# Optimization experiments

Measured on AMD Instinct MI355X. Metric: run time of the kernel, lower is better.

## Reference

```python
import jax, jax.numpy as jnp
import numpy as np

N_NODES = 50000
N_EDGES = 800000
D = 128
H = 8
HD = D // H
N_NTYPES = 3
N_ETYPES = 5
LN_EPS = 1e-5


def setup_inputs() -> dict:
    key = jax.random.key(0)
    ks = jax.random.split(key, 16)
    inp = {
        "x": jax.random.normal(ks[0], (N_NODES, D), dtype=jnp.float32),
        "edge_index": jax.random.randint(ks[1], (2, N_EDGES), 0, N_NODES),
        "edge_type": jax.random.randint(ks[2], (N_EDGES,), 0, N_ETYPES),
        "node_type": jax.random.randint(ks[3], (N_NODES,), 0, N_NTYPES),
        # per-(node_type, head) QKV projections, per-(edge_type, head) K transform
        "W_Q": jax.random.normal(ks[4], (N_NTYPES, H, HD, HD), dtype=jnp.float32) * 0.02,
        "W_K": jax.random.normal(ks[5], (N_NTYPES, H, HD, HD), dtype=jnp.float32) * 0.02,
        "W_V": jax.random.normal(ks[6], (N_NTYPES, H, HD, HD), dtype=jnp.float32) * 0.02,
        "W_edge": jax.random.normal(ks[7], (N_ETYPES, H, HD, HD), dtype=jnp.float32) * 0.02,
        "mu": jnp.ones((H, N_ETYPES), dtype=jnp.float32),
        "W_out": jax.random.normal(ks[8], (D, D), dtype=jnp.float32) * 0.02,
        "b_out": jnp.zeros((D,), dtype=jnp.float32),
        "ln1_g": jnp.ones((D,), dtype=jnp.float32),
        "ln1_b": jnp.zeros((D,), dtype=jnp.float32),
        "W1": jax.random.normal(ks[9], (D, 4 * D), dtype=jnp.float32) * 0.02,
        "b1": jnp.zeros((4 * D,), dtype=jnp.float32),
        "W2": jax.random.normal(ks[10], (4 * D, D), dtype=jnp.float32) * 0.02,
        "b2": jnp.zeros((D,), dtype=jnp.float32),
        "ln2_g": jnp.ones((D,), dtype=jnp.float32),
        "ln2_b": jnp.zeros((D,), dtype=jnp.float32),
    }
    return inp


def _layer_norm(y, g, b):
    m = y.mean(-1, keepdims=True)
    v = ((y - m) ** 2).mean(-1, keepdims=True)
    return (y - m) * jax.lax.rsqrt(v + LN_EPS) * g + b


def reference(x, edge_index, edge_type, node_type,
              W_Q, W_K, W_V, W_edge, mu,
              W_out, b_out, ln1_g, ln1_b, W1, b1, W2, b2, ln2_g, ln2_b):
    N = x.shape[0]
    xh = x.reshape(N, H, HD)  # heads vectorized (concat of per-head slices)

    # type-specific QKV: small fixed loop over node types, masked select
    Q = jnp.zeros_like(xh)
    K = jnp.zeros_like(xh)
    V = jnp.zeros_like(xh)
    for t in range(N_NTYPES):
        m = (node_type == t)[:, None, None]
        Q = jnp.where(m, jnp.einsum('nhd,hdf->nhf', xh, W_Q[t]), Q)
        K = jnp.where(m, jnp.einsum('nhd,hdf->nhf', xh, W_K[t]), K)
        V = jnp.where(m, jnp.einsum('nhd,hdf->nhf', xh, W_V[t]), V)

    src, dst = edge_index[0], edge_index[1]
    q_dst = Q[dst]   # [E,H,HD]
    k_src = K[src]   # [E,H,HD]

    # edge-type-specific K transform
    kt = jnp.zeros_like(k_src)
    for et in range(N_ETYPES):
        m = (edge_type == et)[:, None, None]
        kt = jnp.where(m, jnp.einsum('ehd,hdf->ehf', k_src, W_edge[et]), kt)

    scores = (q_dst * kt).sum(-1) / jnp.sqrt(jnp.float32(HD))  # [E,H]
    scores = scores * mu[:, edge_type].T                       # mu per edge type, per head

    # sparse softmax over incoming edges of each dst node, per head
    smax = jax.ops.segment_max(scores, dst, num_segments=N)
    ex = jnp.exp(scores - smax[dst])
    den = jax.ops.segment_sum(ex, dst, num_segments=N)
    w = ex / (den[dst] + 1e-10)                                 # [E,H]

    agg = jax.ops.segment_sum(V[src] * w[..., None], dst, num_segments=N)  # [N,H,HD]
    mh = agg.reshape(N, D) @ W_out + b_out  # dropout is identity in eval

    h = _layer_norm(x + mh, ln1_g, ln1_b)
    ffn = jax.nn.gelu(h @ W1 + b1, approximate=False) @ W2 + b2
    return _layer_norm(h + ffn, ln2_g, ln2_b)
```

## Files before the change

### kernel.cpp

```cpp
#include <hip/hip_runtime.h>
#include <hip/hip_bf16.h>

#define N_NODESC 50000
#define N_EDGESC 800000
#define DD 128
#define HH 8
#define HDIM 16
#define N_NT 3
#define N_ET 5
#define NPB 196
#define NEB 400
#define NFB 512

#define KV8_OFF    ((size_t)0)
#define QT8_OFF    ((size_t)12800000)
#define XP_OFF     ((size_t)44800000)
#define AGG_OFF    ((size_t)57600000)
#define WOUTT_OFF  ((size_t)83200000)
#define W1T_OFF    ((size_t)83232768)
#define W2T_OFF    ((size_t)83363840)
#define WALL_OFF   ((size_t)83494912)
#define EDATA_OFF  ((size_t)84183040)
#define ROWS_OFF   ((size_t)87383040)
#define ORIG_OFF   ((size_t)87583104)
#define DEG_OFF    ((size_t)87783104)
#define TOFS_OFF   ((size_t)87983104)
#define BH_OFF     ((size_t)87983168)
#define BB_OFF     ((size_t)87985536)
#define TMP_OFF    ((size_t)87988928)
#define RLOC_OFF   ((size_t)91188928)
#define CSUM_OFF   ((size_t)91389056)

using short8 = __attribute__((ext_vector_type(8))) short;
using f32x4  = __attribute__((ext_vector_type(4))) float;
using f32x2  = __attribute__((ext_vector_type(2))) float;

__device__ __forceinline__ ushort f2b(float f) {
    __hip_bfloat16 h = __float2bfloat16(f);
    return *(ushort*)&h;
}
__device__ __forceinline__ float b2f(ushort u) {
    __hip_bfloat16 h = *(__hip_bfloat16*)&u;
    return __bfloat162float(h);
}
__device__ __forceinline__ f32x2 pk0(unsigned int w) {
    return __builtin_amdgcn_cvt_pk_f32_fp8((int)w, false);
}
__device__ __forceinline__ f32x2 pk1(unsigned int w) {
    return __builtin_amdgcn_cvt_pk_f32_fp8((int)w, true);
}
__device__ __forceinline__ float gelu_f(float v) {
    return 0.5f * v * (1.f + erff(v * 0.70710678118654752f));
}
__device__ __forceinline__ void ebar() {
    __builtin_amdgcn_sched_barrier(0);
    asm volatile("s_waitcnt lgkmcnt(0)" ::: "memory");
    __builtin_amdgcn_sched_barrier(0);
    __builtin_amdgcn_s_barrier();
    __builtin_amdgcn_sched_barrier(0);
}

__global__ __launch_bounds__(256) void prep_a(
    const float* __restrict__ Wout, const float* __restrict__ W1, const float* __restrict__ W2,
    const float* __restrict__ WQ, const float* __restrict__ Wk, const float* __restrict__ Wv,
    const float* __restrict__ We, const float* __restrict__ mu,
    ushort* __restrict__ Woutt, ushort* __restrict__ W1t, ushort* __restrict__ W2t,
    ushort* __restrict__ Wall,
    const int* __restrict__ ntype, int* __restrict__ bh,
    const int* __restrict__ dst, int* __restrict__ deg, unsigned int* __restrict__ tmp)
{
    const int b = blockIdx.x, tid = threadIdx.x;
    if (b < 1920) {
        const int gid = b * 256 + tid;
        if (gid < 16384) {
            const int nn = gid >> 7, k = gid & 127;
            Woutt[gid] = f2b(Wout[k * 128 + nn]);
        } else if (gid < 81920) {
            const int i = gid - 16384;
            const int nn = i >> 7, k = i & 127;
            W1t[i] = f2b(W1[k * 512 + nn]);
        } else if (gid < 147456) {
            const int i = gid - 81920;
            const int nn = i >> 9, k = i & 511;
            W2t[i] = f2b(W2[k * 128 + nn]);
        } else {
            const int idx = gid - 147456;
            const int t = idx / (896 * 128);
            const int rem = idx % (896 * 128);
            const int c = rem / 128, k = rem % 128;
            const int hk = k >> 4, ck = k & 15;
            float v = 0.f;
            if (c < 128) {
                const int hc = c >> 4, j = c & 15;
                if (hk == hc) v = 4.f * Wk[((t * HH + hc) * HDIM + ck) * HDIM + j];
            } else if (c < 256) {
                const int c2 = c - 128, hc = c2 >> 4, j = c2 & 15;
                if (hk == hc) v = 4.f * Wv[((t * HH + hc) * HDIM + ck) * HDIM + j];
            } else {
                const int cq = c - 256, et = cq >> 7, dd = cq & 127;
                const int hq = dd >> 4, j = dd & 15;
                if (hk == hq) {
                    const float* wq = WQ + ((t * HH + hq) * HDIM + ck) * HDIM;
                    const float* we = We + ((et * HH + hq) * HDIM + j) * HDIM;
                    float s = 0.f;
#pragma unroll
                    for (int f = 0; f < 16; f++) s = fmaf(wq[f], we[f], s);
                    v = 64.f * mu[hq * N_ET + et] * s;
                }
            }
            Wall[idx] = f2b(v);
        }
    } else if (b < 1920 + NPB) {
        const int bc = b - 1920;
        const int wave = tid >> 6, lane = tid & 63;
        const int n = bc * 256 + tid;
        const int t = (n < N_NODESC) ? ntype[n] : -1;
        const unsigned long long m0 = __ballot(t == 0);
        const unsigned long long m1 = __ballot(t == 1);
        const unsigned long long m2 = __ballot(t == 2);
        __shared__ int wcnt[4][3];
        if (lane == 0) {
            wcnt[wave][0] = (int)__popcll(m0);
            wcnt[wave][1] = (int)__popcll(m1);
            wcnt[wave][2] = (int)__popcll(m2);
        }
        __syncthreads();
        if (tid < 3)
            bh[tid * NPB + bc] = wcnt[0][tid] + wcnt[1][tid] + wcnt[2][tid] + wcnt[3][tid];
    } else {
        for (int e = (b - 1920 - NPB) * 256 + tid; e < N_EDGESC; e += NEB * 256) {
            const int nd = dst[e];
            const unsigned int p = (unsigned int)atomicAdd(&deg[nd], 1);
            tmp[e] = (p << 16) | (unsigned int)nd;
        }
    }
}

__global__ __launch_bounds__(256) void prep_b(
    const int* __restrict__ bh, const int* __restrict__ deg,
    int* __restrict__ bb, int* __restrict__ tofs,
    int* __restrict__ rloc, int* __restrict__ csum)
{
    __shared__ int part[256];
    const int tid = threadIdx.x;
    if (blockIdx.x == 0) {
        const int base3 = tid * 3;
        int e0 = (base3 + 0 < 588) ? bh[base3 + 0] : 0;
        int e1 = (base3 + 1 < 588) ? bh[base3 + 1] : 0;
        int e2 = (base3 + 2 < 588) ? bh[base3 + 2] : 0;
        const int l0 = e0, l1 = e0 + e1, l2 = l1 + e2;
        part[tid] = l2;
        __syncthreads();
        for (int off = 1; off < 256; off <<= 1) {
            const int u = (tid >= off) ? part[tid - off] : 0;
            __syncthreads();
            part[tid] += u;
            __syncthreads();
        }
        const int tb = part[tid] - l2;
        if (base3 + 0 < 588) bb[base3 + 0] = tb;
        if (base3 + 1 < 588) bb[base3 + 1] = tb + l0;
        if (base3 + 2 < 588) bb[base3 + 2] = tb + l1;
        __syncthreads();
        if (tid == 0) {
            tofs[0] = 0;
            tofs[1] = bb[NPB];
            tofs[2] = bb[2 * NPB];
            tofs[3] = N_NODESC;
        }
    } else {
        const int c = blockIdx.x - 1;
        const int n = c * 256 + tid;
        const int vdeg = (n < N_NODESC) ? deg[n] : 0;
        part[tid] = vdeg;
        __syncthreads();
        for (int off = 1; off < 256; off <<= 1) {
            const int u = (tid >= off) ? part[tid - off] : 0;
            __syncthreads();
            part[tid] += u;
            __syncthreads();
        }
        if (n <= N_NODESC) rloc[n] = part[tid] - vdeg;
        if (tid == 255) csum[c] = part[255];
    }
}

__global__ __launch_bounds__(256) void prep_c(
    const int* __restrict__ ntype, const float* __restrict__ x,
    const int* __restrict__ src, const int* __restrict__ etype,
    const int* __restrict__ bb, const int* __restrict__ rloc, const int* __restrict__ csum,
    const unsigned int* __restrict__ tmp,
    int* __restrict__ origof, ushort* __restrict__ Xp, int* __restrict__ rows,
    int* __restrict__ edata)
{
    const int b = blockIdx.x, tid = threadIdx.x;
    __shared__ int cb[256];
    {
        const int v = (tid < NPB) ? csum[tid] : 0;
        cb[tid] = v;
        __syncthreads();
        for (int off = 1; off < 256; off <<= 1) {
            const int u = (tid >= off) ? cb[tid - off] : 0;
            __syncthreads();
            cb[tid] += u;
            __syncthreads();
        }
        const int incl = cb[tid];
        __syncthreads();
        cb[tid] = incl - v;
        __syncthreads();
    }

    if (b < NPB) {
        const int wave = tid >> 6, lane = tid & 63;
        const int n = b * 256 + tid;
        const int t = (n < N_NODESC) ? ntype[n] : -1;
        const unsigned long long m0 = __ballot(t == 0);
        const unsigned long long m1 = __ballot(t == 1);
        const unsigned long long m2 = __ballot(t == 2);
        __shared__ int wcnt[4][3];
        __shared__ int sp[256];
        if (lane == 0) {
            wcnt[wave][0] = (int)__popcll(m0);
            wcnt[wave][1] = (int)__popcll(m1);
            wcnt[wave][2] = (int)__popcll(m2);
        }
        __syncthreads();
        int p = -1;
        if (n < N_NODESC) {
            int basew = 0;
#pragma unroll
            for (int w = 0; w < 4; w++) if (w < wave) basew += wcnt[w][t];
            const unsigned long long mt = (t == 0) ? m0 : (t == 1) ? m1 : m2;
            const unsigned long long mlt = ((unsigned long long)1 << lane) - 1;
            p = bb[t * NPB + b] + basew + (int)__popcll(mt & mlt);
            origof[p] = n;
        }
        if (n <= N_NODESC) rows[n] = cb[b] + rloc[n];
        sp[tid] = p;
        __syncthreads();
        for (int i = tid; i < 256 * 16; i += 256) {
            const int nn = i >> 4, c = (i & 15) << 3;
            const int pp = sp[nn];
            if (pp < 0) continue;
            const int n2 = b * 256 + nn;
            const float4 v0 = *(const float4*)(x + (size_t)n2 * DD + c);
            const float4 v1 = *(const float4*)(x + (size_t)n2 * DD + c + 4);
            ushort o[8] = {f2b(v0.x), f2b(v0.y), f2b(v0.z), f2b(v0.w),
                           f2b(v1.x), f2b(v1.y), f2b(v1.z), f2b(v1.w)};
            *(uint4*)(Xp + (size_t)pp * DD + c) = *(uint4*)o;
        }
    } else {
        for (int e = (b - NPB) * 256 + tid; e < N_EDGESC; e += NFB * 256) {
            const unsigned int v = tmp[e];
            const int nd = (int)(v & 0xffffu);
            const int p = (int)(v >> 16);
            edata[cb[nd >> 8] + rloc[nd] + p] = src[e] | (etype[e] << 16);
        }
    }
}

#define LDP 36

__global__ __launch_bounds__(256) void proj_gemm(
    const ushort* __restrict__ Xp, const ushort* __restrict__ Wall,
    const int* __restrict__ tofs, const int* __restrict__ origof,
    ushort* __restrict__ KV8, unsigned char* __restrict__ Qt8)
{
    const int t = blockIdx.z;
    const int rs = tofs[t], re = tofs[t + 1];
    const int mBase = rs + blockIdx.x * 128;
    if (mBase >= re) return;
    const int nBase = blockIdx.y * 128;
    const ushort* Bt = Wall + (size_t)t * 896 * 128;

    __shared__ ushort As[128 * LDP];
    __shared__ ushort Bs[128 * LDP];
    const int tid = threadIdx.x;
    const int lane = tid & 63, wave = tid >> 6;
    const int mw = (wave >> 1) * 64, nw = (wave & 1) * 64;
    const int l15 = lane & 15, q8 = (lane >> 4) * 8;

    f32x4 acc[4][4];
#pragma unroll
    for (int i = 0; i < 4; i++)
#pragma unroll
        for (int j = 0; j < 4; j++) acc[i][j] = (f32x4){0.f, 0.f, 0.f, 0.f};

    const int r0 = tid >> 2, c0 = (tid & 3) * 8;
    int rA0 = mBase + r0;      if (rA0 >= N_NODESC) rA0 = N_NODESC - 1;
    int rA1 = mBase + r0 + 64; if (rA1 >= N_NODESC) rA1 = N_NODESC - 1;

    for (int kk = 0; kk < 128; kk += 32) {
        short8 a0 = *(const short8*)(Xp + (size_t)rA0 * DD + kk + c0);
        short8 a1 = *(const short8*)(Xp + (size_t)rA1 * DD + kk + c0);
        short8 b0 = *(const short8*)(Bt + (size_t)(nBase + r0) * 128 + kk + c0);
        short8 b1 = *(const short8*)(Bt + (size_t)(nBase + r0 + 64) * 128 + kk + c0);
        *(short8*)&As[r0 * LDP + c0] = a0;
        *(short8*)&As[(r0 + 64) * LDP + c0] = a1;
        *(short8*)&Bs[r0 * LDP + c0] = b0;
        *(short8*)&Bs[(r0 + 64) * LDP + c0] = b1;
        __syncthreads();
        short8 af[4], bf[4];
#pragma unroll
        for (int i = 0; i < 4; i++)
            af[i] = *(const short8*)&As[(mw + i * 16 + l15) * LDP + q8];
#pragma unroll
        for (int j = 0; j < 4; j++)
            bf[j] = *(const short8*)&Bs[(nw + j * 16 + l15) * LDP + q8];
#pragma unroll
        for (int i = 0; i < 4; i++)
#pragma unroll
            for (int j = 0; j < 4; j++)
                acc[i][j] = __builtin_amdgcn_mfma_f32_16x16x32_bf16(af[i], bf[j], acc[i][j], 0, 0, 0);
        __syncthreads();
    }

    unsigned char* kvb = (unsigned char*)KV8;
    const int rq = (lane >> 4) * 4;
#pragma unroll
    for (int i = 0; i < 4; i++) {
#pragma unroll
        for (int r = 0; r < 4; r++) {
            const int gm = mBase + mw + i * 16 + rq + r;
            if (gm >= re) continue;
            const int og = origof[gm];
#pragma unroll
            for (int j = 0; j < 4; j++) {
                const int gn = nBase + nw + j * 16 + l15;
                const float v = acc[i][j][r];
                const unsigned char b8 =
                    (unsigned char)(__builtin_amdgcn_cvt_pk_fp8_f32(v, v, 0, false) & 0xff);
                if (gn < 256) kvb[(size_t)og * 256 + gn] = b8;
                else          Qt8[(size_t)og * 640 + (gn - 256)] = b8;
            }
        }
    }
}

__global__ __launch_bounds__(128) void edgeagg_kernel(
    const int* __restrict__ rowstart, const int* __restrict__ edata,
    const unsigned char* __restrict__ Qt8, const unsigned char* __restrict__ KV8,
    ushort* __restrict__ agg)
{
    const int w = threadIdx.x >> 6;
    const int lane = threadIdx.x & 63;
    const int n = blockIdx.x * 2 + w;
    const int slot = lane >> 3;
    const int h = lane & 7;

    __shared__ uint4 qs8s[2][40];
    if (lane < 40)
        qs8s[w][lane] = ((const uint4*)(Qt8 + (size_t)n * 640))[lane];
    __syncthreads();
    const uint* qbase = (const uint*)&qs8s[w][0];

    const int s0 = rowstart[n], s1 = rowstart[n + 1];
    const float qsc = 1.44269504f / 1024.f;

    float acc[16];
#pragma unroll
    for (int j = 0; j < 16; j++) acc[j] = 0.f;
    float den = 0.f;

    for (int i = s0 + slot; i < s1; i += 8) {
        const int ed = edata[i];
        const int sn = ed & 0xffff;
        const int et = ed >> 16;
        const unsigned char* kvp = KV8 + ((size_t)sn << 8);
        const uint4 kw = *(const uint4*)(kvp + (h << 4));
        const uint4 vw = *(const uint4*)(kvp + 128 + (h << 4));
        const uint4 qw = *(const uint4*)(qbase + (et << 5) + (h << 2));

        const f32x2 q0 = pk0(qw.x), q1 = pk1(qw.x), q2 = pk0(qw.y), q3 = pk1(qw.y);
        const f32x2 q4 = pk0(qw.z), q5 = pk1(qw.z), q6 = pk0(qw.w), q7 = pk1(qw.w);
        const f32x2 k0 = pk0(kw.x), k1 = pk1(kw.x), k2 = pk0(kw.y), k3 = pk1(kw.y);
        const f32x2 k4 = pk0(kw.z), k5 = pk1(kw.z), k6 = pk0(kw.w), k7 = pk1(kw.w);

        float pa = q0.x * k0.x;
        float pb = q0.y * k0.y;
        float pc = q1.x * k1.x;
        float pd = q1.y * k1.y;
        pa = fmaf(q2.x, k2.x, pa); pb = fmaf(q2.y, k2.y, pb);
        pc = fmaf(q3.x, k3.x, pc); pd = fmaf(q3.y, k3.y, pd);
        pa = fmaf(q4.x, k4.x, pa); pb = fmaf(q4.y, k4.y, pb);
        pc = fmaf(q5.x, k5.x, pc); pd = fmaf(q5.y, k5.y, pd);
        pa = fmaf(q6.x, k6.x, pa); pb = fmaf(q6.y, k6.y, pb);
        pc = fmaf(q7.x, k7.x, pc); pd = fmaf(q7.y, k7.y, pd);

        const float ex = exp2f(((pa + pb) + (pc + pd)) * qsc);
        den += ex;

        const f32x2 v0 = pk0(vw.x), v1 = pk1(vw.x), v2 = pk0(vw.y), v3 = pk1(vw.y);
        const f32x2 v4 = pk0(vw.z), v5 = pk1(vw.z), v6 = pk0(vw.w), v7 = pk1(vw.w);
        acc[0]  = fmaf(ex, v0.x, acc[0]);  acc[1]  = fmaf(ex, v0.y, acc[1]);
        acc[2]  = fmaf(ex, v1.x, acc[2]);  acc[3]  = fmaf(ex, v1.y, acc[3]);
        acc[4]  = fmaf(ex, v2.x, acc[4]);  acc[5]  = fmaf(ex, v2.y, acc[5]);
        acc[6]  = fmaf(ex, v3.x, acc[6]);  acc[7]  = fmaf(ex, v3.y, acc[7]);
        acc[8]  = fmaf(ex, v4.x, acc[8]);  acc[9]  = fmaf(ex, v4.y, acc[9]);
        acc[10] = fmaf(ex, v5.x, acc[10]); acc[11] = fmaf(ex, v5.y, acc[11]);
        acc[12] = fmaf(ex, v6.x, acc[12]); acc[13] = fmaf(ex, v6.y, acc[13]);
        acc[14] = fmaf(ex, v7.x, acc[14]); acc[15] = fmaf(ex, v7.y, acc[15]);
    }

    {
        const int b0 = slot & 1, b1 = slot & 2, b2 = slot & 4;
#pragma unroll
        for (int j = 0; j < 8; j++) {
            const float v = b0 ? acc[j] : acc[j + 8];
            const float r = __shfl_xor(v, 8);
            acc[j] = (b0 ? acc[j + 8] : acc[j]) + r;
        }
#pragma unroll
        for (int j = 0; j < 4; j++) {
            const float v = b1 ? acc[j] : acc[j + 4];
            const float r = __shfl_xor(v, 16);
            acc[j] = (b1 ? acc[j + 4] : acc[j]) + r;
        }
#pragma unroll
        for (int j = 0; j < 2; j++) {
            const float v = b2 ? acc[j] : acc[j + 2];
            const float r = __shfl_xor(v, 32);
            acc[j] = (b2 ? acc[j + 2] : acc[j]) + r;
        }
        den += __shfl_xor(den, 8);
        den += __shfl_xor(den, 16);
        den += __shfl_xor(den, 32);
    }
    const float rr = 0.25f / (den + 1e-10f);
    const int fb = (h << 4) + ((slot & 1) << 3) + ((slot & 2) << 1) + ((slot & 4) >> 1);
    ushort o2[2] = { f2b(acc[0] * rr), f2b(acc[1] * rr) };
    *(uint*)&agg[((size_t)n << 7) + fb] = *(uint*)o2;
}

#define LDH 132
#define LDB 132

__global__ __launch_bounds__(256) void fused_tail(
    const ushort* __restrict__ agg, const ushort* __restrict__ Woutt,
    const ushort* __restrict__ W1t, const ushort* __restrict__ W2t,
    const float* __restrict__ x,
    const float* __restrict__ bout, const float* __restrict__ g1, const float* __restrict__ b1ln,
    const float* __restrict__ b1, const float* __restrict__ b2,
    const float* __restrict__ g2, const float* __restrict__ b2ln,
    float* __restrict__ out)
{
    __shared__ ushort Bs[128 * LDB];
    __shared__ ushort Hs[64 * LDH];
    __shared__ ushort Ts[64 * LDH];
    __shared__ float red[2][2][64];

    const int tid = threadIdx.x;
    const int lane = tid & 63, wave = tid >> 6;
    const int wm = wave >> 1, wn = wave & 1;
    const int l15 = lane & 15, q8 = (lane >> 4) * 8, rq = (lane >> 4) * 4;
    const int mBase = blockIdx.x * 64;

    const int r0 = tid >> 2, c0 = (tid & 3) * 8;
    int rowA = mBase + r0; if (rowA >= N_NODESC) rowA = N_NODESC - 1;

    short8 pA[4], pB0[4], pB1[4];
#pragma unroll
    for (int kk = 0; kk < 4; kk++) {
        pA[kk]  = *(const short8*)(agg + (size_t)rowA * DD + kk * 32 + c0);
        pB0[kk] = *(const short8*)(Woutt + (size_t)r0 * 128 + kk * 32 + c0);
        pB1[kk] = *(const short8*)(Woutt + (size_t)(r0 + 64) * 128 + kk * 32 + c0);
    }
    float xv[2][4][4];
#pragma unroll
    for (int i = 0; i < 2; i++)
#pragma unroll
        for (int r = 0; r < 4; r++) {
            const int gm = mBase + wm * 32 + i * 16 + rq + r;
            const int gr = (gm < N_NODESC) ? gm : N_NODESC - 1;
#pragma unroll
            for (int j = 0; j < 4; j++)
                xv[i][r][j] = x[(size_t)gr * DD + wn * 64 + j * 16 + l15];
        }

    f32x4 acc1[2][4], acc2[2][4];
#pragma unroll
    for (int i = 0; i < 2; i++)
#pragma unroll
        for (int j = 0; j < 4; j++) {
            acc1[i][j] = (f32x4){0.f, 0.f, 0.f, 0.f};
            acc2[i][j] = (f32x4){0.f, 0.f, 0.f, 0.f};
        }

#pragma unroll
    for (int kk = 0; kk < 4; kk++) {
        *(short8*)&Ts[r0 * LDH + kk * 32 + c0] = pA[kk];
        *(short8*)&Bs[r0 * LDB + kk * 32 + c0] = pB0[kk];
        *(short8*)&Bs[(r0 + 64) * LDB + kk * 32 + c0] = pB1[kk];
    }
#pragma unroll
    for (int kk = 0; kk < 4; kk++) {
        pB0[kk] = *(const short8*)(W1t + (size_t)r0 * 128 + kk * 32 + c0);
        pB1[kk] = *(const short8*)(W1t + (size_t)(r0 + 64) * 128 + kk * 32 + c0);
    }
    ebar();
#pragma unroll
    for (int kk = 0; kk < 4; kk++) {
        short8 af[2], bf[4];
#pragma unroll
        for (int i = 0; i < 2; i++)
            af[i] = *(const short8*)&Ts[(wm * 32 + i * 16 + l15) * LDH + kk * 32 + q8];
#pragma unroll
        for (int j = 0; j < 4; j++)
            bf[j] = *(const short8*)&Bs[(wn * 64 + j * 16 + l15) * LDB + kk * 32 + q8];
#pragma unroll
        for (int i = 0; i < 2; i++)
#pragma unroll
            for (int j = 0; j < 4; j++)
                acc1[i][j] = __builtin_amdgcn_mfma_f32_16x16x32_bf16(af[i], bf[j], acc1[i][j], 0, 0, 0);
    }

    {
        float boutv[4], gv[4], bv[4];
#pragma unroll
        for (int j = 0; j < 4; j++) {
            const int gn = wn * 64 + j * 16 + l15;
            boutv[j] = bout[gn]; gv[j] = g1[gn]; bv[j] = b1ln[gn];
        }
#pragma unroll
        for (int i = 0; i < 2; i++) {
#pragma unroll
            for (int r = 0; r < 4; r++) {
                const int row = wm * 32 + i * 16 + rq + r;
                float s = 0.f, ss = 0.f;
#pragma unroll
                for (int j = 0; j < 4; j++) {
                    float v = acc1[i][j][r] + boutv[j] + xv[i][r][j];
                    acc1[i][j][r] = v;
                    s += v; ss += v * v;
                }
                s  += __shfl_xor(s, 1);  s  += __shfl_xor(s, 2);  s  += __shfl_xor(s, 4);  s  += __shfl_xor(s, 8);
                ss += __shfl_xor(ss, 1); ss += __shfl_xor(ss, 2); ss += __shfl_xor(ss, 4); ss += __shfl_xor(ss, 8);
                if (l15 == 0) { red[0][wn][row] = s; red[1][wn][row] = ss; }
            }
        }
        ebar();
#pragma unroll
        for (int i = 0; i < 2; i++) {
#pragma unroll
            for (int r = 0; r < 4; r++) {
                const int row = wm * 32 + i * 16 + rq + r;
                const float s  = red[0][0][row] + red[0][1][row];
                const float ss = red[1][0][row] + red[1][1][row];
                const float mean = s * (1.f / 128.f);
                const float var  = ss * (1.f / 128.f) - mean * mean;
                const float rstd = rsqrtf(var + 1e-5f);
#pragma unroll
                for (int j = 0; j < 4; j++) {
                    const int gn = wn * 64 + j * 16 + l15;
                    Hs[row * LDH + gn] = f2b((acc1[i][j][r] - mean) * rstd * gv[j] + bv[j]);
                }
            }
        }
    }

    for (int nb = 0; nb < 4; nb++) {
        ebar();
#pragma unroll
        for (int kk = 0; kk < 4; kk++) {
            *(short8*)&Bs[r0 * LDB + kk * 32 + c0] = pB0[kk];
            *(short8*)&Bs[(r0 + 64) * LDB + kk * 32 + c0] = pB1[kk];
        }
#pragma unroll
        for (int kk = 0; kk < 4; kk++) {
            pB0[kk] = *(const short8*)(W2t + (size_t)r0 * 512 + nb * 128 + kk * 32 + c0);
            pB1[kk] = *(const short8*)(W2t + (size_t)(r0 + 64) * 512 + nb * 128 + kk * 32 + c0);
        }
        ebar();
        f32x4 a1[2][4];
#pragma unroll
        for (int i = 0; i < 2; i++)
#pragma unroll
            for (int j = 0; j < 4; j++) a1[i][j] = (f32x4){0.f, 0.f, 0.f, 0.f};
#pragma unroll
        for (int kk = 0; kk < 4; kk++) {
            short8 af[2], bf[4];
#pragma unroll
            for (int i = 0; i < 2; i++)
                af[i] = *(const short8*)&Hs[(wm * 32 + i * 16 + l15) * LDH + kk * 32 + q8];
#pragma unroll
            for (int j = 0; j < 4; j++)
                bf[j] = *(const short8*)&Bs[(wn * 64 + j * 16 + l15) * LDB + kk * 32 + q8];
#pragma unroll
            for (int i = 0; i < 2; i++)
#pragma unroll
                for (int j = 0; j < 4; j++)
                    a1[i][j] = __builtin_amdgcn_mfma_f32_16x16x32_bf16(af[i], bf[j], a1[i][j], 0, 0, 0);
        }

        ebar();
        {
            float b1v[4];
#pragma unroll
            for (int j = 0; j < 4; j++)
                b1v[j] = b1[nb * 128 + wn * 64 + j * 16 + l15];
#pragma unroll
            for (int i = 0; i < 2; i++)
#pragma unroll
                for (int j = 0; j < 4; j++)
#pragma unroll
                    for (int r = 0; r < 4; r++) {
                        const int row = wm * 32 + i * 16 + rq + r;
                        const int col = wn * 64 + j * 16 + l15;
                        Ts[row * LDH + col] = f2b(gelu_f(a1[i][j][r] + b1v[j]));
                    }
        }
#pragma unroll
        for (int kk = 0; kk < 4; kk++) {
            *(short8*)&Bs[r0 * LDB + kk * 32 + c0] = pB0[kk];
            *(short8*)&Bs[(r0 + 64) * LDB + kk * 32 + c0] = pB1[kk];
        }
        if (nb < 3) {
#pragma unroll
            for (int kk = 0; kk < 4; kk++) {
                pB0[kk] = *(const short8*)(W1t + (size_t)((nb + 1) * 128 + r0) * 128 + kk * 32 + c0);
                pB1[kk] = *(const short8*)(W1t + (size_t)((nb + 1) * 128 + r0 + 64) * 128 + kk * 32 + c0);
            }
        }
        ebar();
#pragma unroll
        for (int kk = 0; kk < 4; kk++) {
            short8 af[2], bf[4];
#pragma unroll
            for (int i = 0; i < 2; i++)
                af[i] = *(const short8*)&Ts[(wm * 32 + i * 16 + l15) * LDH + kk * 32 + q8];
#pragma unroll
            for (int j = 0; j < 4; j++)
                bf[j] = *(const short8*)&Bs[(wn * 64 + j * 16 + l15) * LDB + kk * 32 + q8];
#pragma unroll
            for (int i = 0; i < 2; i++)
#pragma unroll
                for (int j = 0; j < 4; j++)
                    acc2[i][j] = __builtin_amdgcn_mfma_f32_16x16x32_bf16(af[i], bf[j], acc2[i][j], 0, 0, 0);
        }
    }

    {
        float b2v[4], gv[4], bv[4];
#pragma unroll
        for (int j = 0; j < 4; j++) {
            const int gn = wn * 64 + j * 16 + l15;
            b2v[j] = b2[gn]; gv[j] = g2[gn]; bv[j] = b2ln[gn];
        }
#pragma unroll
        for (int i = 0; i < 2; i++) {
#pragma unroll
            for (int r = 0; r < 4; r++) {
                const int row = wm * 32 + i * 16 + rq + r;
                float s = 0.f, ss = 0.f;
#pragma unroll
                for (int j = 0; j < 4; j++) {
                    const int gn = wn * 64 + j * 16 + l15;
                    float v = acc2[i][j][r] + b2v[j] + b2f(Hs[row * LDH + gn]);
                    acc2[i][j][r] = v;
                    s += v; ss += v * v;
                }
                s  += __shfl_xor(s, 1);  s  += __shfl_xor(s, 2);  s  += __shfl_xor(s, 4);  s  += __shfl_xor(s, 8);
                ss += __shfl_xor(ss, 1); ss += __shfl_xor(ss, 2); ss += __shfl_xor(ss, 4); ss += __shfl_xor(ss, 8);
                if (l15 == 0) { red[0][wn][row] = s; red[1][wn][row] = ss; }
            }
        }
        ebar();
#pragma unroll
        for (int i = 0; i < 2; i++) {
#pragma unroll
            for (int r = 0; r < 4; r++) {
                const int row = wm * 32 + i * 16 + rq + r;
                const int gm = mBase + row;
                if (gm >= N_NODESC) continue;
                const float s  = red[0][0][row] + red[0][1][row];
                const float ss = red[1][0][row] + red[1][1][row];
                const float mean = s * (1.f / 128.f);
                const float var  = ss * (1.f / 128.f) - mean * mean;
                const float rstd = rsqrtf(var + 1e-5f);
#pragma unroll
                for (int j = 0; j < 4; j++) {
                    const int gn = wn * 64 + j * 16 + l15;
                    out[(size_t)gm * DD + gn] = (acc2[i][j][r] - mean) * rstd * gv[j] + bv[j];
                }
            }
        }
    }
}

extern "C" void kernel_launch(void* const* d_in, const int* in_sizes, int n_in,
                              void* d_out, int out_size, void* d_ws, size_t ws_size,
                              hipStream_t stream)
{
    const float* x     = (const float*)d_in[0];
    const int*   ei    = (const int*)d_in[1];
    const int*   etyp  = (const int*)d_in[2];
    const int*   ntype = (const int*)d_in[3];
    const float* Wq    = (const float*)d_in[4];
    const float* Wk    = (const float*)d_in[5];
    const float* Wv    = (const float*)d_in[6];
    const float* We    = (const float*)d_in[7];
    const float* mu    = (const float*)d_in[8];
    const float* Wout  = (const float*)d_in[9];
    const float* bout  = (const float*)d_in[10];
    const float* g1    = (const float*)d_in[11];
    const float* b1ln  = (const float*)d_in[12];
    const float* W1    = (const float*)d_in[13];
    const float* b1    = (const float*)d_in[14];
    const float* W2    = (const float*)d_in[15];
    const float* b2    = (const float*)d_in[16];
    const float* g2    = (const float*)d_in[17];
    const float* b2ln  = (const float*)d_in[18];
    float* out = (float*)d_out;

    char* ws = (char*)d_ws;
    ushort*        KV8   = (ushort*)(ws + KV8_OFF);
    unsigned char* Qt8   = (unsigned char*)(ws + QT8_OFF);
    ushort*        Xp    = (ushort*)(ws + XP_OFF);
    ushort*        agg   = (ushort*)(ws + AGG_OFF);
    ushort*        Woutt = (ushort*)(ws + WOUTT_OFF);
    ushort*        W1t   = (ushort*)(ws + W1T_OFF);
    ushort*        W2t   = (ushort*)(ws + W2T_OFF);
    ushort*        Wall  = (ushort*)(ws + WALL_OFF);
    int*           edata = (int*)(ws + EDATA_OFF);
    int*           rows  = (int*)(ws + ROWS_OFF);
    int*           origof= (int*)(ws + ORIG_OFF);
    int*           deg   = (int*)(ws + DEG_OFF);
    int*           tofs  = (int*)(ws + TOFS_OFF);
    int*           bh    = (int*)(ws + BH_OFF);
    int*           bb    = (int*)(ws + BB_OFF);
    unsigned int*  tmp   = (unsigned int*)(ws + TMP_OFF);
    int*           rloc  = (int*)(ws + RLOC_OFF);
    int*           csum  = (int*)(ws + CSUM_OFF);

    const int* srcA = ei;
    const int* dstA = ei + N_EDGESC;

    (void)hipMemsetAsync(ws + DEG_OFF, 0, 200000, stream);

    prep_a<<<1920 + NPB + NEB, 256, 0, stream>>>(
        Wout, W1, W2, Wq, Wk, Wv, We, mu, Woutt, W1t, W2t, Wall,
        ntype, bh, dstA, deg, tmp);
    prep_b<<<1 + NPB, 256, 0, stream>>>(bh, deg, bb, tofs, rloc, csum);
    prep_c<<<NPB + NFB, 256, 0, stream>>>(ntype, x, srcA, etyp, bb, rloc, csum, tmp,
                                          origof, Xp, rows, edata);

    proj_gemm<<<dim3(394, 7, 3), 256, 0, stream>>>(Xp, Wall, tofs, origof, KV8, Qt8);
    edgeagg_kernel<<<N_NODESC / 2, 128, 0, stream>>>(rows, edata, Qt8,
                                                     (const unsigned char*)KV8, agg);

    fused_tail<<<782, 256, 0, stream>>>(agg, Woutt, W1t, W2t, x,
                                        bout, g1, b1ln, b1, b2, g2, b2ln, out);
}
```

Baseline: 317.7 us.

## Restructure fused tail to 512 threads with K-split double-buffered weights and fast GELU

The fused tail kernel moves from 4 to 8 waves per block, each wave handling a 32x32 output tile. The weight tiles are split into two 64-wide K halves held in a double-buffered LDS array, so global loads of the next half can overlap the MFMA work on the current one. The exact erff in GELU is replaced by an Abramowitz-Stegun polynomial using a hardware reciprocal and a fast exp. This trades extra barriers and an approximation error of about 1e-7 in erf for better latency hiding and occupancy.

```diff
diff --git a/kernel.cpp b/kernel.cpp
--- a/kernel.cpp
+++ b/kernel.cpp
@@ -50,7 +50,20 @@
     return __builtin_amdgcn_cvt_pk_f32_fp8((int)w, true);
 }
 __device__ __forceinline__ float gelu_f(float v) {
-    return 0.5f * v * (1.f + erff(v * 0.70710678118654752f));
+    const float x = v * 0.70710678118654752f;
+    const float ax = fabsf(x);
+    const float d = fmaf(0.3275911f, ax, 1.0f);
+    float t;
+    asm("v_rcp_f32 %0, %1" : "=v"(t) : "v"(d));
+    float p = fmaf(1.061405429f, t, -1.453152027f);
+    p = fmaf(p, t, 1.421413741f);
+    p = fmaf(p, t, -0.284496736f);
+    p = fmaf(p, t, 0.254829592f);
+    p = p * t;
+    const float e = __expf(-ax * ax);
+    const float er = 1.0f - p * e;
+    const float erfx = (x < 0.f) ? -er : er;
+    return 0.5f * v * (1.0f + erfx);
 }
 __device__ __forceinline__ void ebar() {
     __builtin_amdgcn_sched_barrier(0);
@@ -434,9 +447,13 @@
 }
 
 #define LDH 132
-#define LDB 132
-
-__global__ __launch_bounds__(256) void fused_tail(
+#define LDB2 68
+
+#define LOADB(P0, P1, PTR) { P0 = *(const short8*)(PTR); P1 = *(const short8*)((PTR) + 8); }
+#define STAGEB(BUF, P0, P1) { *(short8*)&Bs[BUF][br * LDB2 + bc] = P0; \
+                              *(short8*)&Bs[BUF][br * LDB2 + bc + 8] = P1; }
+
+__global__ __launch_bounds__(512, 4) void fused_tail(
     const ushort* __restrict__ agg, const ushort* __restrict__ Woutt,
     const ushort* __restrict__ W1t, const ushort* __restrict__ W2t,
     const float* __restrict__ x,
@@ -445,28 +462,36 @@
     const float* __restrict__ g2, const float* __restrict__ b2ln,
     float* __restrict__ out)
 {
-    __shared__ ushort Bs[128 * LDB];
+    __shared__ ushort Bs[2][128 * LDB2];
     __shared__ ushort Hs[64 * LDH];
     __shared__ ushort Ts[64 * LDH];
-    __shared__ float red[2][2][64];
+    __shared__ float red[2][4][64];
 
     const int tid = threadIdx.x;
     const int lane = tid & 63, wave = tid >> 6;
-    const int wm = wave >> 1, wn = wave & 1;
+    const int wm = wave >> 2, wn = wave & 3;
     const int l15 = lane & 15, q8 = (lane >> 4) * 8, rq = (lane >> 4) * 4;
     const int mBase = blockIdx.x * 64;
 
-    const int r0 = tid >> 2, c0 = (tid & 3) * 8;
-    int rowA = mBase + r0; if (rowA >= N_NODESC) rowA = N_NODESC - 1;
-
-    short8 pA[4], pB0[4], pB1[4];
-#pragma unroll
-    for (int kk = 0; kk < 4; kk++) {
-        pA[kk]  = *(const short8*)(agg + (size_t)rowA * DD + kk * 32 + c0);
-        pB0[kk] = *(const short8*)(Woutt + (size_t)r0 * 128 + kk * 32 + c0);
-        pB1[kk] = *(const short8*)(Woutt + (size_t)(r0 + 64) * 128 + kk * 32 + c0);
-    }
-    float xv[2][4][4];
+    const int br = tid >> 2, bc = (tid & 3) * 16;
+    const int ar = tid >> 3, ac = (tid & 7) * 16;
+    int rowA = mBase + ar; if (rowA >= N_NODESC) rowA = N_NODESC - 1;
+
+    f32x4 acc1[2][2], acc2[2][2];
+#pragma unroll
+    for (int i = 0; i < 2; i++)
+#pragma unroll
+        for (int j = 0; j < 2; j++) {
+            acc1[i][j] = (f32x4){0.f, 0.f, 0.f, 0.f};
+            acc2[i][j] = (f32x4){0.f, 0.f, 0.f, 0.f};
+        }
+
+    short8 pX0, pX1, pY0, pY1, aT0, aT1;
+    LOADB(pX0, pX1, Woutt + (size_t)br * 128 + bc);
+    LOADB(pY0, pY1, Woutt + (size_t)br * 128 + 64 + bc);
+    aT0 = *(const short8*)(agg + (size_t)rowA * DD + ac);
+    aT1 = *(const short8*)(agg + (size_t)rowA * DD + ac + 8);
+    float xv[2][4][2];
 #pragma unroll
     for (int i = 0; i < 2; i++)
 #pragma unroll
@@ -474,53 +499,59 @@
             const int gm = mBase + wm * 32 + i * 16 + rq + r;
             const int gr = (gm < N_NODESC) ? gm : N_NODESC - 1;
 #pragma unroll
-            for (int j = 0; j < 4; j++)
-                xv[i][r][j] = x[(size_t)gr * DD + wn * 64 + j * 16 + l15];
-        }
-
-    f32x4 acc1[2][4], acc2[2][4];
-#pragma unroll
-    for (int i = 0; i < 2; i++)
-#pragma unroll
-        for (int j = 0; j < 4; j++) {
-            acc1[i][j] = (f32x4){0.f, 0.f, 0.f, 0.f};
-            acc2[i][j] = (f32x4){0.f, 0.f, 0.f, 0.f};
-        }
-
-#pragma unroll
-    for (int kk = 0; kk < 4; kk++) {
-        *(short8*)&Ts[r0 * LDH + kk * 32 + c0] = pA[kk];
-        *(short8*)&Bs[r0 * LDB + kk * 32 + c0] = pB0[kk];
-        *(short8*)&Bs[(r0 + 64) * LDB + kk * 32 + c0] = pB1[kk];
-    }
-#pragma unroll
-    for (int kk = 0; kk < 4; kk++) {
-        pB0[kk] = *(const short8*)(W1t + (size_t)r0 * 128 + kk * 32 + c0);
-        pB1[kk] = *(const short8*)(W1t + (size_t)(r0 + 64) * 128 + kk * 32 + c0);
-    }
+            for (int j = 0; j < 2; j++)
+                xv[i][r][j] = x[(size_t)gr * DD + wn * 32 + j * 16 + l15];
+        }
+    *(short8*)&Ts[ar * LDH + ac] = aT0;
+    *(short8*)&Ts[ar * LDH + ac + 8] = aT1;
+    STAGEB(0, pX0, pX1);
+    LOADB(pX0, pX1, W1t + (size_t)br * 128 + bc);
     ebar();
-#pragma unroll
-    for (int kk = 0; kk < 4; kk++) {
-        short8 af[2], bf[4];
+
+    STAGEB(1, pY0, pY1);
+    LOADB(pY0, pY1, W1t + (size_t)br * 128 + 64 + bc);
+#pragma unroll
+    for (int kk2 = 0; kk2 < 2; kk2++) {
+        short8 af[2], bf[2];
 #pragma unroll
         for (int i = 0; i < 2; i++)
-            af[i] = *(const short8*)&Ts[(wm * 32 + i * 16 + l15) * LDH + kk * 32 + q8];
-#pragma unroll
-        for (int j = 0; j < 4; j++)
-            bf[j] = *(const short8*)&Bs[(wn * 64 + j * 16 + l15) * LDB + kk * 32 + q8];
+            af[i] = *(const short8*)&Ts[(wm * 32 + i * 16 + l15) * LDH + kk2 * 32 + q8];
+#pragma unroll
+        for (int j = 0; j < 2; j++)
+            bf[j] = *(const short8*)&Bs[0][(wn * 32 + j * 16 + l15) * LDB2 + kk2 * 32 + q8];
 #pragma unroll
         for (int i = 0; i < 2; i++)
 #pragma unroll
-            for (int j = 0; j < 4; j++)
+            for (int j = 0; j < 2; j++)
                 acc1[i][j] = __builtin_amdgcn_mfma_f32_16x16x32_bf16(af[i], bf[j], acc1[i][j], 0, 0, 0);
     }
+    ebar();
+
+    STAGEB(0, pX0, pX1);
+    LOADB(pX0, pX1, W2t + (size_t)br * 512 + bc);
+#pragma unroll
+    for (int kk2 = 0; kk2 < 2; kk2++) {
+        short8 af[2], bf[2];
+#pragma unroll
+        for (int i = 0; i < 2; i++)
+            af[i] = *(const short8*)&Ts[(wm * 32 + i * 16 + l15) * LDH + 64 + kk2 * 32 + q8];
+#pragma unroll
+        for (int j = 0; j < 2; j++)
+            bf[j] = *(const short8*)&Bs[1][(wn * 32 + j * 16 + l15) * LDB2 + kk2 * 32 + q8];
+#pragma unroll
+        for (int i = 0; i < 2; i++)
+#pragma unroll
+            for (int j = 0; j < 2; j++)
+                acc1[i][j] = __builtin_amdgcn_mfma_f32_16x16x32_bf16(af[i], bf[j], acc1[i][j], 0, 0, 0);
+    }
+    ebar();
 
     {
-        float boutv[4], gv[4], bv[4];
-#pragma unroll
-        for (int j = 0; j < 4; j++) {
-            const int gn = wn * 64 + j * 16 + l15;
-            boutv[j] = bout[gn]; gv[j] = g1[gn]; bv[j] = b1ln[gn];
+        float bo[2], gv[2], bv[2];
+#pragma unroll
+        for (int j = 0; j < 2; j++) {
+            const int gn = wn * 32 + j * 16 + l15;
+            bo[j] = bout[gn]; gv[j] = g1[gn]; bv[j] = b1ln[gn];
         }
 #pragma unroll
         for (int i = 0; i < 2; i++) {
@@ -529,8 +560,8 @@
                 const int row = wm * 32 + i * 16 + rq + r;
                 float s = 0.f, ss = 0.f;
 #pragma unroll
-                for (int j = 0; j < 4; j++) {
-                    float v = acc1[i][j][r] + boutv[j] + xv[i][r][j];
+                for (int j = 0; j < 2; j++) {
+                    float v = acc1[i][j][r] + bo[j] + xv[i][r][j];
                     acc1[i][j][r] = v;
                     s += v; ss += v * v;
                 }
@@ -545,106 +576,130 @@
 #pragma unroll
             for (int r = 0; r < 4; r++) {
                 const int row = wm * 32 + i * 16 + rq + r;
-                const float s  = red[0][0][row] + red[0][1][row];
-                const float ss = red[1][0][row] + red[1][1][row];
+                const float s  = red[0][0][row] + red[0][1][row] + red[0][2][row] + red[0][3][row];
+                const float ss = red[1][0][row] + red[1][1][row] + red[1][2][row] + red[1][3][row];
                 const float mean = s * (1.f / 128.f);
                 const float var  = ss * (1.f / 128.f) - mean * mean;
                 const float rstd = rsqrtf(var + 1e-5f);
 #pragma unroll
-                for (int j = 0; j < 4; j++) {
-                    const int gn = wn * 64 + j * 16 + l15;
+                for (int j = 0; j < 2; j++) {
+                    const int gn = wn * 32 + j * 16 + l15;
                     Hs[row * LDH + gn] = f2b((acc1[i][j][r] - mean) * rstd * gv[j] + bv[j]);
                 }
             }
         }
+        ebar();
     }
 
     for (int nb = 0; nb < 4; nb++) {
+        f32x4 a1[2][2];
+#pragma unroll
+        for (int i = 0; i < 2; i++)
+#pragma unroll
+            for (int j = 0; j < 2; j++) a1[i][j] = (f32x4){0.f, 0.f, 0.f, 0.f};
+
+        STAGEB(1, pY0, pY1);
+        LOADB(pY0, pY1, W2t + (size_t)br * 512 + nb * 128 + 64 + bc);
+#pragma unroll
+        for (int kk2 = 0; kk2 < 2; kk2++) {
+            short8 af[2], bf[2];
+#pragma unroll
+            for (int i = 0; i < 2; i++)
+                af[i] = *(const short8*)&Hs[(wm * 32 + i * 16 + l15) * LDH + kk2 * 32 + q8];
+#pragma unroll
+            for (int j = 0; j < 2; j++)
+                bf[j] = *(const short8*)&Bs[0][(wn * 32 + j * 16 + l15) * LDB2 + kk2 * 32 + q8];
+#pragma unroll
+            for (int i = 0; i < 2; i++)
+#pragma unroll
+                for (int j = 0; j < 2; j++)
+                    a1[i][j] = __builtin_amdgcn_mfma_f32_16x16x32_bf16(af[i], bf[j], a1[i][j], 0, 0, 0);
+        }
         ebar();
-#pragma unroll
-        for (int kk = 0; kk < 4; kk++) {
-            *(short8*)&Bs[r0 * LDB + kk * 32 + c0] = pB0[kk];
-            *(short8*)&Bs[(r0 + 64) * LDB + kk * 32 + c0] = pB1[kk];
-        }
-#pragma unroll
-        for (int kk = 0; kk < 4; kk++) {
-            pB0[kk] = *(const short8*)(W2t + (size_t)r0 * 512 + nb * 128 + kk * 32 + c0);
-            pB1[kk] = *(const short8*)(W2t + (size_t)(r0 + 64) * 512 + nb * 128 + kk * 32 + c0);
+
+        STAGEB(0, pX0, pX1);
+        if (nb < 3) { LOADB(pX0, pX1, W1t + (size_t)((nb + 1) * 128 + br) * 128 + bc); }
+#pragma unroll
+        for (int kk2 = 0; kk2 < 2; kk2++) {
+            short8 af[2], bf[2];
+#pragma unroll
+            for (int i = 0; i < 2; i++)
+                af[i] = *(const short8*)&Hs[(wm * 32 + i * 16 + l15) * LDH + 64 + kk2 * 32 + q8];
+#pragma unroll
+            for (int j = 0; j < 2; j++)
+                bf[j] = *(const short8*)&Bs[1][(wn * 32 + j * 16 + l15) * LDB2 + kk2 * 32 + q8];
+#pragma unroll
+            for (int i = 0; i < 2; i++)
+#pragma unroll
+                for (int j = 0; j < 2; j++)
+                    a1[i][j] = __builtin_amdgcn_mfma_f32_16x16x32_bf16(af[i], bf[j], a1[i][j], 0, 0, 0);
         }
         ebar();
-        f32x4 a1[2][4];
-#pragma unroll
-        for (int i = 0; i < 2; i++)
-#pragma unroll
-            for (int j = 0; j < 4; j++) a1[i][j] = (f32x4){0.f, 0.f, 0.f, 0.f};
-#pragma unroll
-        for (int kk = 0; kk < 4; kk++) {
-            short8 af[2], bf[4];
+
+        {
+            float b1v[2];
+#pragma unroll
+            for (int j = 0; j < 2; j++)
+                b1v[j] = b1[nb * 128 + wn * 32 + j * 16 + l15];
 #pragma unroll
             for (int i = 0; i < 2; i++)
-                af[i] = *(const short8*)&Hs[(wm * 32 + i * 16 + l15) * LDH + kk * 32 + q8];
-#pragma unroll
-            for (int j = 0; j < 4; j++)
-                bf[j] = *(const short8*)&Bs[(wn * 64 + j * 16 + l15) * LDB + kk * 32 + q8];
-#pragma unroll
-            for (int i = 0; i < 2; i++)
-#pragma unroll
-                for (int j = 0; j < 4; j++)
-                    a1[i][j] = __builtin_amdgcn_mfma_f32_16x16x32_bf16(af[i], bf[j], a1[i][j], 0, 0, 0);
-        }
-
-        ebar();
-        {
-            float b1v[4];
-#pragma unroll
-            for (int j = 0; j < 4; j++)
-                b1v[j] = b1[nb * 128 + wn * 64 + j * 16 + l15];
-#pragma unroll
-            for (int i = 0; i < 2; i++)
-#pragma unroll
-                for (int j = 0; j < 4; j++)
+#pragma unroll
+                for (int j = 0; j < 2; j++)
 #pragma unroll
                     for (int r = 0; r < 4; r++) {
                         const int row = wm * 32 + i * 16 + rq + r;
-                        const int col = wn * 64 + j * 16 + l15;
+                        const int col = wn * 32 + j * 16 + l15;
                         Ts[row * LDH + col] = f2b(gelu_f(a1[i][j][r] + b1v[j]));
                     }
         }
-#pragma unroll
-        for (int kk = 0; kk < 4; kk++) {
-            *(short8*)&Bs[r0 * LDB + kk * 32 + c0] = pB0[kk];
-            *(short8*)&Bs[(r0 + 64) * LDB + kk * 32 + c0] = pB1[kk];
-        }
+        ebar();
+
+        STAGEB(1, pY0, pY1);
+        if (nb < 3) { LOADB(pY0, pY1, W1t + (size_t)((nb + 1) * 128 + br) * 128 + 64 + bc); }
+#pragma unroll
+        for (int kk2 = 0; kk2 < 2; kk2++) {
+            short8 af[2], bf[2];
+#pragma unroll
+            for (int i = 0; i < 2; i++)
+                af[i] = *(const short8*)&Ts[(wm * 32 + i * 16 + l15) * LDH + kk2 * 32 + q8];
+#pragma unroll
+            for (int j = 0; j < 2; j++)
+                bf[j] = *(const short8*)&Bs[0][(wn * 32 + j * 16 + l15) * LDB2 + kk2 * 32 + q8];
+#pragma unroll
+            for (int i = 0; i < 2; i++)
+#pragma unroll
+                for (int j = 0; j < 2; j++)
+                    acc2[i][j] = __builtin_amdgcn_mfma_f32_16x16x32_bf16(af[i], bf[j], acc2[i][j], 0, 0, 0);
+        }
+        ebar();
+
         if (nb < 3) {
-#pragma unroll
-            for (int kk = 0; kk < 4; kk++) {
-                pB0[kk] = *(const short8*)(W1t + (size_t)((nb + 1) * 128 + r0) * 128 + kk * 32 + c0);
-                pB1[kk] = *(const short8*)(W1t + (size_t)((nb + 1) * 128 + r0 + 64) * 128 + kk * 32 + c0);
-            }
+            STAGEB(0, pX0, pX1);
+            LOADB(pX0, pX1, W2t + (size_t)br * 512 + (nb + 1) * 128 + bc);
+        }
+#pragma unroll
+        for (int kk2 = 0; kk2 < 2; kk2++) {
+            short8 af[2], bf[2];
+#pragma unroll
+            for (int i = 0; i < 2; i++)
+                af[i] = *(const short8*)&Ts[(wm * 32 + i * 16 + l15) * LDH + 64 + kk2 * 32 + q8];
+#pragma unroll
+            for (int j = 0; j < 2; j++)
+                bf[j] = *(const short8*)&Bs[1][(wn * 32 + j * 16 + l15) * LDB2 + kk2 * 32 + q8];
+#pragma unroll
+            for (int i = 0; i < 2; i++)
+#pragma unroll
+                for (int j = 0; j < 2; j++)
+                    acc2[i][j] = __builtin_amdgcn_mfma_f32_16x16x32_bf16(af[i], bf[j], acc2[i][j], 0, 0, 0);
         }
         ebar();
-#pragma unroll
-        for (int kk = 0; kk < 4; kk++) {
-            short8 af[2], bf[4];
-#pragma unroll
-            for (int i = 0; i < 2; i++)
-                af[i] = *(const short8*)&Ts[(wm * 32 + i * 16 + l15) * LDH + kk * 32 + q8];
-#pragma unroll
-            for (int j = 0; j < 4; j++)
-                bf[j] = *(const short8*)&Bs[(wn * 64 + j * 16 + l15) * LDB + kk * 32 + q8];
-#pragma unroll
-            for (int i = 0; i < 2; i++)
-#pragma unroll
-                for (int j = 0; j < 4; j++)
-                    acc2[i][j] = __builtin_amdgcn_mfma_f32_16x16x32_bf16(af[i], bf[j], acc2[i][j], 0, 0, 0);
-        }
     }
 
     {
-        float b2v[4], gv[4], bv[4];
-#pragma unroll
-        for (int j = 0; j < 4; j++) {
-            const int gn = wn * 64 + j * 16 + l15;
+        float b2v[2], gv[2], bv[2];
+#pragma unroll
+        for (int j = 0; j < 2; j++) {
+            const int gn = wn * 32 + j * 16 + l15;
             b2v[j] = b2[gn]; gv[j] = g2[gn]; bv[j] = b2ln[gn];
         }
 #pragma unroll
@@ -654,8 +709,8 @@
                 const int row = wm * 32 + i * 16 + rq + r;
                 float s = 0.f, ss = 0.f;
 #pragma unroll
-                for (int j = 0; j < 4; j++) {
-                    const int gn = wn * 64 + j * 16 + l15;
+                for (int j = 0; j < 2; j++) {
+                    const int gn = wn * 32 + j * 16 + l15;
                     float v = acc2[i][j][r] + b2v[j] + b2f(Hs[row * LDH + gn]);
                     acc2[i][j][r] = v;
                     s += v; ss += v * v;
@@ -673,14 +728,14 @@
                 const int row = wm * 32 + i * 16 + rq + r;
                 const int gm = mBase + row;
                 if (gm >= N_NODESC) continue;
-                const float s  = red[0][0][row] + red[0][1][row];
-                const float ss = red[1][0][row] + red[1][1][row];
+                const float s  = red[0][0][row] + red[0][1][row] + red[0][2][row] + red[0][3][row];
+                const float ss = red[1][0][row] + red[1][1][row] + red[1][2][row] + red[1][3][row];
                 const float mean = s * (1.f / 128.f);
                 const float var  = ss * (1.f / 128.f) - mean * mean;
                 const float rstd = rsqrtf(var + 1e-5f);
 #pragma unroll
-                for (int j = 0; j < 4; j++) {
-                    const int gn = wn * 64 + j * 16 + l15;
+                for (int j = 0; j < 2; j++) {
+                    const int gn = wn * 32 + j * 16 + l15;
                     out[(size_t)gm * DD + gn] = (acc2[i][j][r] - mean) * rstd * gv[j] + bv[j];
                 }
             }
@@ -749,6 +804,6 @@
     edgeagg_kernel<<<N_NODESC / 2, 128, 0, stream>>>(rows, edata, Qt8,
                                                      (const unsigned char*)KV8, agg);
 
-    fused_tail<<<782, 256, 0, stream>>>(agg, Woutt, W1t, W2t, x,
+    fused_tail<<<782, 512, 0, stream>>>(agg, Woutt, W1t, W2t, x,
                                         bout, g1, b1ln, b1, b2, g2, b2ln, out);
 }
```

Result: no change. 322.3 us (+1.5%).
